# Performance work log

Measured on AMD Instinct MI355X. Metric: run time of the kernel, lower is better.

The kernel has to match this reference:

```python
import jax, jax.numpy as jnp
import numpy as np

B, N, M = 8, 4096, 4096


def setup_inputs() -> dict:
    key = jax.random.key(0)
    ks = jax.random.split(key, 8)
    return {
        "x_aligned": jax.random.normal(ks[0], (B, N, 3), dtype=jnp.float32),
        "y": jax.random.normal(ks[1], (B, M, 3), dtype=jnp.float32),
        "R": jax.random.normal(ks[2], (B, 3, 3), dtype=jnp.float32),
        "S": jax.random.normal(ks[3], (B, 3), dtype=jnp.float32),
        "t": jax.random.normal(ks[4], (B, 3, 1), dtype=jnp.float32),
        "R_gt": jax.random.normal(ks[5], (B, 3, 3), dtype=jnp.float32),
        "S_gt": jax.random.normal(ks[6], (B, 3), dtype=jnp.float32),
        "t_gt": jax.random.normal(ks[7], (B, 3), dtype=jnp.float32),
    }


def chamfer_distance(x, y):
    # x: [B,N,3], y: [B,M,3]; bidirectional mean squared NN distance
    xn = jnp.sum(x * x, axis=-1)                      # [B,N]
    yn = jnp.sum(y * y, axis=-1)                      # [B,M]
    xy = jnp.einsum('bnd,bmd->bnm', x, y)             # [B,N,M]
    d2 = xn[:, :, None] + yn[:, None, :] - 2.0 * xy   # [B,N,M] squared dists
    cham_x = jnp.mean(jnp.min(d2, axis=2), axis=1)    # [B] x -> y
    cham_y = jnp.mean(jnp.min(d2, axis=1), axis=1)    # [B] y -> x
    return jnp.mean(cham_x) + jnp.mean(cham_y)        # batch mean, summed dirs


def reference(x_aligned, y, R, S, t, R_gt, S_gt, t_gt):
    t = jnp.squeeze(t)                                # [B,3]
    eye = jnp.eye(3, dtype=R.dtype)
    R_loss = jnp.einsum('bij,bkj->bik', R, R_gt) - eye  # R @ R_gt^T - I
    L_reg = (jnp.sum(R_loss * R_loss)
             + jnp.sum((S - S_gt) ** 2)
             + jnp.sum((t - t_gt) ** 2))
    L_chamfer = chamfer_distance(x_aligned, y)
    return L_reg + L_chamfer
```

## Files before the change

### kernel.cpp

```cpp
#include <hip/hip_runtime.h>

#define BB 8
#define NN 4096
#define MC 256
#define NCHUNK (NN / MC)
#define KPT 4
#define TPB 256
#define PTS_PER_BLOCK (TPB * KPT)
#define NPTS (2 * BB * NN)


__global__ __launch_bounds__(TPB) void chamfer_partial(
    const float* __restrict__ X, const float* __restrict__ Y,
    float* __restrict__ partial, float* __restrict__ out) {
  __shared__ float4 ly[MC];
  const int tid = threadIdx.x;
  const int zb  = blockIdx.z;
  const int b   = zb & (BB - 1);
  const int dir = zb >> 3;
  const float* pts  = dir ? (Y + b * NN * 3) : (X + b * NN * 3);
  const float* refs = dir ? (X + b * NN * 3) : (Y + b * NN * 3);
  const int c = blockIdx.y;

  if (tid == 0 && blockIdx.x == 0 && blockIdx.y == 0 && blockIdx.z == 0)
    *out = 0.0f;

  {
    const int j = c * MC + tid;
    const float a0 = refs[j * 3 + 0];
    const float a1 = refs[j * 3 + 1];
    const float a2 = refs[j * 3 + 2];
    ly[tid] = make_float4(-2.0f * a0, -2.0f * a1, -2.0f * a2,
                          a0 * a0 + a1 * a1 + a2 * a2);
  }
  __syncthreads();

  float px[KPT], py[KPT], pz[KPT], m[KPT];
  const int p0 = blockIdx.x * PTS_PER_BLOCK + tid;
#pragma unroll
  for (int k = 0; k < KPT; k++) {
    const int p = p0 + k * TPB;
    px[k] = pts[p * 3 + 0];
    py[k] = pts[p * 3 + 1];
    pz[k] = pts[p * 3 + 2];
    m[k] = 1e30f;
  }

#define CHAMFER_BODY(w0, w1, w2, w3)                                           \
  _Pragma("unroll") for (int k = 0; k < KPT; k++) {                            \
    const float s0 =                                                           \
        fmaf(px[k], w0.x, fmaf(py[k], w0.y, fmaf(pz[k], w0.z, w0.w)));         \
    const float s1 =                                                           \
        fmaf(px[k], w1.x, fmaf(py[k], w1.y, fmaf(pz[k], w1.z, w1.w)));         \
    const float s2 =                                                           \
        fmaf(px[k], w2.x, fmaf(py[k], w2.y, fmaf(pz[k], w2.z, w2.w)));         \
    const float s3 =                                                           \
        fmaf(px[k], w3.x, fmaf(py[k], w3.y, fmaf(pz[k], w3.z, w3.w)));         \
    m[k] = fminf(m[k], fminf(fminf(s0, s1), fminf(s2, s3)));                   \
  }

  float4 w0 = ly[0], w1 = ly[1], w2 = ly[2], w3 = ly[3];
#pragma unroll 2
  for (int j = 0; j < MC - 4; j += 4) {
    const float4 n0 = ly[j + 4];
    const float4 n1 = ly[j + 5];
    const float4 n2 = ly[j + 6];
    const float4 n3 = ly[j + 7];
    CHAMFER_BODY(w0, w1, w2, w3)
    w0 = n0; w1 = n1; w2 = n2; w3 = n3;
  }
  CHAMFER_BODY(w0, w1, w2, w3)
#undef CHAMFER_BODY

#pragma unroll
  for (int k = 0; k < KPT; k++) {
    const int p = p0 + k * TPB;
    const float pn = px[k] * px[k] + py[k] * py[k] + pz[k] * pz[k];
    partial[(c * (2 * BB) + zb) * NN + p] = m[k] + pn;
  }
}

__global__ __launch_bounds__(256) void chamfer_reduce(
    const float* __restrict__ partial,
    const float* __restrict__ R, const float* __restrict__ S,
    const float* __restrict__ t, const float* __restrict__ Rgt,
    const float* __restrict__ Sgt, const float* __restrict__ tgt,
    float* __restrict__ out) {
  const int tid = threadIdx.x;
  const int q = blockIdx.x * 256 + tid;
  float m = 1e30f;
#pragma unroll
  for (int c = 0; c < NCHUNK; c++)
    m = fminf(m, partial[c * NPTS + q]);
  float s = m;
  for (int o = 32; o > 0; o >>= 1) s += __shfl_down(s, o);
  __shared__ float wsum[4];
  if ((tid & 63) == 0) wsum[tid >> 6] = s;
  __syncthreads();
  if (tid == 0) {
    const float bs = wsum[0] + wsum[1] + wsum[2] + wsum[3];
    atomicAdd(out, bs * (1.0f / (float)(BB * NN)));
  }

  if (blockIdx.x == 0) {
    float v = 0.0f;
    if (tid < 72) {
      const int b = tid / 9, ik = tid % 9, i = ik / 3, k = ik % 3;
      const float* Rb = R + b * 9;
      const float* Gb = Rgt + b * 9;
      float d = Rb[i * 3 + 0] * Gb[k * 3 + 0] +
                Rb[i * 3 + 1] * Gb[k * 3 + 1] +
                Rb[i * 3 + 2] * Gb[k * 3 + 2];
      d -= (i == k) ? 1.0f : 0.0f;
      v = d * d;
    } else if (tid < 96) {
      const int i = tid - 72;
      const float d = S[i] - Sgt[i];
      v = d * d;
    } else if (tid < 120) {
      const int i = tid - 96;
      const float d = t[i] - tgt[i];
      v = d * d;
    }
    for (int o = 32; o > 0; o >>= 1) v += __shfl_down(v, o);
    __shared__ float rsum[4];
    if ((tid & 63) == 0) rsum[tid >> 6] = v;
    __syncthreads();
    if (tid == 0) atomicAdd(out, rsum[0] + rsum[1] + rsum[2] + rsum[3]);
  }
}

extern "C" void kernel_launch(void* const* d_in, const int* in_sizes, int n_in,
                              void* d_out, int out_size, void* d_ws, size_t ws_size,
                              hipStream_t stream) {
  const float* X   = (const float*)d_in[0];
  const float* Y   = (const float*)d_in[1];
  const float* R   = (const float*)d_in[2];
  const float* S   = (const float*)d_in[3];
  const float* t   = (const float*)d_in[4];
  const float* Rgt = (const float*)d_in[5];
  const float* Sgt = (const float*)d_in[6];
  const float* tgt = (const float*)d_in[7];

  float* partial = (float*)d_ws;
  float* out     = (float*)d_out;

  dim3 gA(NN / PTS_PER_BLOCK, NCHUNK, 2 * BB);
  chamfer_partial<<<gA, TPB, 0, stream>>>(X, Y, partial, out);

  chamfer_reduce<<<NPTS / 256, 256, 0, stream>>>(partial, R, S, t, Rgt, Sgt, tgt, out);
}
```

Before: 91.46 us.

## Fuse chamfer partial and reduce kernels via cooperative grid sync, double chunk size

Merges the partial nearest-neighbour kernel and the reduction kernel into one cooperative launch separated by a grid-wide sync, so the second kernel launch goes away. The reference chunk size grows from 256 to 512, which halves the number of chunks and partial rows to reduce. It also splits the min into two dependent fminf steps. In exchange it takes on the cost of a grid barrier, a cooperative launch limited by how many blocks can be co-resident (4x8x16=512 blocks), and larger shared memory per block.

```diff
diff --git a/kernel.cpp b/kernel.cpp
--- a/kernel.cpp
+++ b/kernel.cpp
@@ -1,17 +1,24 @@
 #include <hip/hip_runtime.h>
+#include <hip/hip_cooperative_groups.h>
+
+namespace cg = cooperative_groups;
 
 #define BB 8
 #define NN 4096
-#define MC 256
+#define MC 512
 #define NCHUNK (NN / MC)
 #define KPT 4
 #define TPB 256
 #define PTS_PER_BLOCK (TPB * KPT)
+#define GRID_X (NN / PTS_PER_BLOCK)
 #define NPTS (2 * BB * NN)
 
 
-__global__ __launch_bounds__(TPB) void chamfer_partial(
+__global__ __launch_bounds__(TPB) void hegn_fused(
     const float* __restrict__ X, const float* __restrict__ Y,
+    const float* __restrict__ R, const float* __restrict__ S,
+    const float* __restrict__ t, const float* __restrict__ Rgt,
+    const float* __restrict__ Sgt, const float* __restrict__ tgt,
     float* __restrict__ partial, float* __restrict__ out) {
   __shared__ float4 ly[MC];
   const int tid = threadIdx.x;
@@ -25,13 +32,15 @@
   if (tid == 0 && blockIdx.x == 0 && blockIdx.y == 0 && blockIdx.z == 0)
     *out = 0.0f;
 
-  {
-    const int j = c * MC + tid;
+#pragma unroll
+  for (int i = 0; i < MC / TPB; i++) {
+    const int jj = i * TPB + tid;
+    const int j = c * MC + jj;
     const float a0 = refs[j * 3 + 0];
     const float a1 = refs[j * 3 + 1];
     const float a2 = refs[j * 3 + 2];
-    ly[tid] = make_float4(-2.0f * a0, -2.0f * a1, -2.0f * a2,
-                          a0 * a0 + a1 * a1 + a2 * a2);
+    ly[jj] = make_float4(-2.0f * a0, -2.0f * a1, -2.0f * a2,
+                         a0 * a0 + a1 * a1 + a2 * a2);
   }
   __syncthreads();
 
@@ -56,7 +65,8 @@
         fmaf(px[k], w2.x, fmaf(py[k], w2.y, fmaf(pz[k], w2.z, w2.w)));         \
     const float s3 =                                                           \
         fmaf(px[k], w3.x, fmaf(py[k], w3.y, fmaf(pz[k], w3.z, w3.w)));         \
-    m[k] = fminf(m[k], fminf(fminf(s0, s1), fminf(s2, s3)));                   \
+    m[k] = fminf(fminf(s0, s1), m[k]);                      \
+    m[k] = fminf(fminf(s2, s3), m[k]);                      \
   }
 
   float4 w0 = ly[0], w1 = ly[1], w2 = ly[2], w3 = ly[3];
@@ -78,21 +88,18 @@
     const float pn = px[k] * px[k] + py[k] * py[k] + pz[k] * pz[k];
     partial[(c * (2 * BB) + zb) * NN + p] = m[k] + pn;
   }
-}
 
-__global__ __launch_bounds__(256) void chamfer_reduce(
-    const float* __restrict__ partial,
-    const float* __restrict__ R, const float* __restrict__ S,
-    const float* __restrict__ t, const float* __restrict__ Rgt,
-    const float* __restrict__ Sgt, const float* __restrict__ tgt,
-    float* __restrict__ out) {
-  const int tid = threadIdx.x;
-  const int q = blockIdx.x * 256 + tid;
-  float m = 1e30f;
+  cg::this_grid().sync();
+
+  const int bid = blockIdx.x + GRID_X * (blockIdx.y + NCHUNK * blockIdx.z);
+  if (bid >= 256) return;
+
+  const int q = bid * 256 + tid;
+  float mn = 1e30f;
 #pragma unroll
-  for (int c = 0; c < NCHUNK; c++)
-    m = fminf(m, partial[c * NPTS + q]);
-  float s = m;
+  for (int cc = 0; cc < NCHUNK; cc++)
+    mn = fminf(mn, partial[cc * NPTS + q]);
+  float s = mn;
   for (int o = 32; o > 0; o >>= 1) s += __shfl_down(s, o);
   __shared__ float wsum[4];
   if ((tid & 63) == 0) wsum[tid >> 6] = s;
@@ -102,12 +109,12 @@
     atomicAdd(out, bs * (1.0f / (float)(BB * NN)));
   }
 
-  if (blockIdx.x == 0) {
+  if (bid == 0) {
     float v = 0.0f;
     if (tid < 72) {
-      const int b = tid / 9, ik = tid % 9, i = ik / 3, k = ik % 3;
-      const float* Rb = R + b * 9;
-      const float* Gb = Rgt + b * 9;
+      const int bb = tid / 9, ik = tid % 9, i = ik / 3, k = ik % 3;
+      const float* Rb = R + bb * 9;
+      const float* Gb = Rgt + bb * 9;
       float d = Rb[i * 3 + 0] * Gb[k * 3 + 0] +
                 Rb[i * 3 + 1] * Gb[k * 3 + 1] +
                 Rb[i * 3 + 2] * Gb[k * 3 + 2];
@@ -145,8 +152,10 @@
   float* partial = (float*)d_ws;
   float* out     = (float*)d_out;
 
-  dim3 gA(NN / PTS_PER_BLOCK, NCHUNK, 2 * BB);
-  chamfer_partial<<<gA, TPB, 0, stream>>>(X, Y, partial, out);
-
-  chamfer_reduce<<<NPTS / 256, 256, 0, stream>>>(partial, R, S, t, Rgt, Sgt, tgt, out);
+  dim3 gA(GRID_X, NCHUNK, 2 * BB);
+  void* args[] = {(void*)&X, (void*)&Y, (void*)&R, (void*)&S, (void*)&t,
+                  (void*)&Rgt, (void*)&Sgt, (void*)&tgt,
+                  (void*)&partial, (void*)&out};
+  hipLaunchCooperativeKernel((void*)hegn_fused, gA, dim3(TPB, 1, 1), args, 0,
+                             stream);
 }
```

New measurement: 144.1 us. 1.58x slower.

## Fuse chamfer reduction into main kernel via atomic min and last-block reduction

Applied to the files above, without the earlier changes.

Replaces the partial-min buffer and the separate reduce kernel with order-preserving encoded atomicMax into a per-point min array. A per-direction-batch counter picks the last finishing block, which sums the mins; a second counter picks the final block, which adds the regularisation terms and writes the output. This removes a kernel launch and the round trip through a 16x-larger partial buffer. In exchange it adds a memset, global atomics, and thread fences.

```diff
diff --git a/kernel.cpp b/kernel.cpp
--- a/kernel.cpp
+++ b/kernel.cpp
@@ -7,12 +7,30 @@
 #define KPT 4
 #define TPB 256
 #define PTS_PER_BLOCK (TPB * KPT)
-#define NPTS (2 * BB * NN)
+#define NZB (2 * BB)
+#define NPTS (NZB * NN)
 
+#define WS_ZERO_WORDS (NPTS + NZB + 1)
 
-__global__ __launch_bounds__(TPB) void chamfer_partial(
+__device__ __forceinline__ unsigned enc_min(float v) {
+  const unsigned u = __float_as_uint(v);
+  const unsigned key = (u & 0x80000000u) ? ~u : (u | 0x80000000u);
+  return ~key;
+}
+__device__ __forceinline__ float dec_max(unsigned s) {
+  const unsigned key = ~s;
+  const unsigned u = (key & 0x80000000u) ? (key ^ 0x80000000u) : ~key;
+  return __uint_as_float(u);
+}
+
+__global__ __launch_bounds__(TPB) void hegn_chamfer(
     const float* __restrict__ X, const float* __restrict__ Y,
-    float* __restrict__ partial, float* __restrict__ out) {
+    const float* __restrict__ R, const float* __restrict__ S,
+    const float* __restrict__ t, const float* __restrict__ Rgt,
+    const float* __restrict__ Sgt, const float* __restrict__ tgt,
+    unsigned* __restrict__ mins, unsigned* __restrict__ counters,
+    unsigned* __restrict__ counter2, float* __restrict__ zbsum,
+    float* __restrict__ out) {
   __shared__ float4 ly[MC];
   const int tid = threadIdx.x;
   const int zb  = blockIdx.z;
@@ -21,9 +39,6 @@
   const float* pts  = dir ? (Y + b * NN * 3) : (X + b * NN * 3);
   const float* refs = dir ? (X + b * NN * 3) : (Y + b * NN * 3);
   const int c = blockIdx.y;
-
-  if (tid == 0 && blockIdx.x == 0 && blockIdx.y == 0 && blockIdx.z == 0)
-    *out = 0.0f;
 
   {
     const int j = c * MC + tid;
@@ -76,58 +91,62 @@
   for (int k = 0; k < KPT; k++) {
     const int p = p0 + k * TPB;
     const float pn = px[k] * px[k] + py[k] * py[k] + pz[k] * pz[k];
-    partial[(c * (2 * BB) + zb) * NN + p] = m[k] + pn;
+    atomicMax(&mins[zb * NN + p], enc_min(m[k] + pn));
   }
-}
 
-__global__ __launch_bounds__(256) void chamfer_reduce(
-    const float* __restrict__ partial,
-    const float* __restrict__ R, const float* __restrict__ S,
-    const float* __restrict__ t, const float* __restrict__ Rgt,
-    const float* __restrict__ Sgt, const float* __restrict__ tgt,
-    float* __restrict__ out) {
-  const int tid = threadIdx.x;
-  const int q = blockIdx.x * 256 + tid;
-  float m = 1e30f;
+  __threadfence();
+  __shared__ unsigned is_fin;
+  if (tid == 0) is_fin = (atomicAdd(&counters[zb], 1u) == 63u) ? 1u : 0u;
+  __syncthreads();
+  if (!is_fin) return;
+
+  __threadfence();
+  const uint4* mz = (const uint4*)(mins + zb * NN);
+  float s = 0.0f;
 #pragma unroll
-  for (int c = 0; c < NCHUNK; c++)
-    m = fminf(m, partial[c * NPTS + q]);
-  float s = m;
+  for (int i = 0; i < 4; i++) {
+    const uint4 v = mz[i * TPB + tid];
+    s += (dec_max(v.x) + dec_max(v.y)) + (dec_max(v.z) + dec_max(v.w));
+  }
   for (int o = 32; o > 0; o >>= 1) s += __shfl_down(s, o);
   __shared__ float wsum[4];
   if ((tid & 63) == 0) wsum[tid >> 6] = s;
   __syncthreads();
+  __shared__ unsigned is_last;
   if (tid == 0) {
-    const float bs = wsum[0] + wsum[1] + wsum[2] + wsum[3];
-    atomicAdd(out, bs * (1.0f / (float)(BB * NN)));
+    zbsum[zb] = wsum[0] + wsum[1] + wsum[2] + wsum[3];
+    __threadfence();
+    is_last = (atomicAdd(counter2, 1u) == (unsigned)(NZB - 1)) ? 1u : 0u;
   }
+  __syncthreads();
+  if (!is_last) return;
 
-  if (blockIdx.x == 0) {
-    float v = 0.0f;
-    if (tid < 72) {
-      const int b = tid / 9, ik = tid % 9, i = ik / 3, k = ik % 3;
-      const float* Rb = R + b * 9;
-      const float* Gb = Rgt + b * 9;
-      float d = Rb[i * 3 + 0] * Gb[k * 3 + 0] +
-                Rb[i * 3 + 1] * Gb[k * 3 + 1] +
-                Rb[i * 3 + 2] * Gb[k * 3 + 2];
-      d -= (i == k) ? 1.0f : 0.0f;
-      v = d * d;
-    } else if (tid < 96) {
-      const int i = tid - 72;
-      const float d = S[i] - Sgt[i];
-      v = d * d;
-    } else if (tid < 120) {
-      const int i = tid - 96;
-      const float d = t[i] - tgt[i];
-      v = d * d;
-    }
-    for (int o = 32; o > 0; o >>= 1) v += __shfl_down(v, o);
-    __shared__ float rsum[4];
-    if ((tid & 63) == 0) rsum[tid >> 6] = v;
-    __syncthreads();
-    if (tid == 0) atomicAdd(out, rsum[0] + rsum[1] + rsum[2] + rsum[3]);
+  __threadfence();
+  float v = 0.0f;
+  if (tid < 72) {
+    const int bb = tid / 9, ik = tid % 9, i = ik / 3, k = ik % 3;
+    const float* Rb = R + bb * 9;
+    const float* Gb = Rgt + bb * 9;
+    float d = Rb[i * 3 + 0] * Gb[k * 3 + 0] +
+              Rb[i * 3 + 1] * Gb[k * 3 + 1] +
+              Rb[i * 3 + 2] * Gb[k * 3 + 2];
+    d -= (i == k) ? 1.0f : 0.0f;
+    v = d * d;
+  } else if (tid < 96) {
+    const int i = tid - 72;
+    const float d = S[i] - Sgt[i];
+    v = d * d;
+  } else if (tid < 120) {
+    const int i = tid - 96;
+    const float d = t[i] - tgt[i];
+    v = d * d;
   }
+  if (tid < NZB) v += zbsum[tid] * (1.0f / (float)(BB * NN));
+  for (int o = 32; o > 0; o >>= 1) v += __shfl_down(v, o);
+  __shared__ float rsum[4];
+  if ((tid & 63) == 0) rsum[tid >> 6] = v;
+  __syncthreads();
+  if (tid == 0) *out = rsum[0] + rsum[1] + rsum[2] + rsum[3];
 }
 
 extern "C" void kernel_launch(void* const* d_in, const int* in_sizes, int n_in,
@@ -142,11 +161,15 @@
   const float* Sgt = (const float*)d_in[6];
   const float* tgt = (const float*)d_in[7];
 
-  float* partial = (float*)d_ws;
-  float* out     = (float*)d_out;
+  unsigned* mins     = (unsigned*)d_ws;
+  unsigned* counters = mins + NPTS;
+  unsigned* counter2 = counters + NZB;
+  float*    zbsum    = (float*)(counter2 + 1);
+  float*    out      = (float*)d_out;
 
-  dim3 gA(NN / PTS_PER_BLOCK, NCHUNK, 2 * BB);
-  chamfer_partial<<<gA, TPB, 0, stream>>>(X, Y, partial, out);
+  hipMemsetAsync(d_ws, 0, WS_ZERO_WORDS * sizeof(unsigned), stream);
 
-  chamfer_reduce<<<NPTS / 256, 256, 0, stream>>>(partial, R, S, t, Rgt, Sgt, tgt, out);
+  dim3 gA(NN / PTS_PER_BLOCK, NCHUNK, NZB);
+  hegn_chamfer<<<gA, TPB, 0, stream>>>(X, Y, R, S, t, Rgt, Sgt, tgt,
+                                       mins, counters, counter2, zbsum, out);
 }
```

Measured after the change: 148.7 us. +62.6%, slower.
